# Performance work log

Hardware: AMD Instinct MI355X
Metric: run time of the kernel (lower is better)

## Reference

```python
import jax, jax.numpy as jnp
import numpy as np

N_NODES = 100000
N_EDGES = 3200000
F_IN = 256
HID = 64
N_CLS = 16


def setup_inputs() -> dict:
    key = jax.random.key(0)
    ks = jax.random.split(key, 12)
    x = jax.random.normal(ks[0], (N_NODES, F_IN), dtype=jnp.float32)
    edge_index = jax.random.randint(ks[1], (2, N_EDGES), 0, N_NODES, dtype=jnp.int32)
    w_mul = jax.random.normal(ks[2], (N_EDGES, 1), dtype=jnp.float32)
    s1 = 1.0 / np.sqrt(F_IN)
    s2 = 1.0 / np.sqrt(HID)
    # layer 1 params
    lin1_w = jax.random.uniform(ks[3], (HID, F_IN), minval=-s1, maxval=s1, dtype=jnp.float32)
    lin1_b = jax.random.uniform(ks[4], (HID,), minval=-s1, maxval=s1, dtype=jnp.float32)
    mlp1_w0 = jax.random.uniform(ks[5], (HID, 1), minval=-1.0, maxval=1.0, dtype=jnp.float32)
    mlp1_w1 = jax.random.uniform(ks[6], (HID, HID), minval=-s2, maxval=s2, dtype=jnp.float32)
    mlp1_b1 = jax.random.uniform(ks[7], (HID,), minval=-s2, maxval=s2, dtype=jnp.float32)
    # layer 2 params
    lin2_w = jax.random.uniform(ks[8], (N_CLS, HID), minval=-s2, maxval=s2, dtype=jnp.float32)
    lin2_b = jax.random.uniform(ks[9], (N_CLS,), minval=-s2, maxval=s2, dtype=jnp.float32)
    mlp2_w0 = jax.random.uniform(ks[10], (HID, 1), minval=-1.0, maxval=1.0, dtype=jnp.float32)
    mlp2_w1 = jax.random.uniform(ks[11], (N_CLS, HID), minval=-s2, maxval=s2, dtype=jnp.float32)
    mlp2_b1 = jnp.zeros((N_CLS,), dtype=jnp.float32)
    return dict(x=x, edge_index=edge_index, w_mul=w_mul,
                lin1_w=lin1_w, lin1_b=lin1_b, mlp1_w0=mlp1_w0, mlp1_w1=mlp1_w1, mlp1_b1=mlp1_b1,
                lin2_w=lin2_w, lin2_b=lin2_b, mlp2_w0=mlp2_w0, mlp2_w1=mlp2_w1, mlp2_b1=mlp2_b1)


def curv_layer(x, src, dst, w_mul, lin_w, lin_b, m_w0, m_w1, m_b1, n_nodes):
    # dense projection: [N, out]
    h = x @ lin_w.T + lin_b
    # per-edge weight MLP: Linear(1,HID,no bias) -> LeakyReLU(0.2) -> Linear(HID,out,bias)
    ew = jax.nn.leaky_relu(w_mul @ m_w0.T, negative_slope=0.2) @ m_w1.T + m_b1  # [E, out]
    # segment softmax keyed by source node (PyG softmax(out_weight, edge_index[0]))
    emax = jax.ops.segment_max(ew, src, num_segments=n_nodes)  # [N, out]
    e = jnp.exp(ew - emax[src])
    esum = jax.ops.segment_sum(e, src, num_segments=n_nodes)
    alpha = e / (esum[src] + 1e-16)  # [E, out]
    # message = alpha * x_j (x_j = h[src]); scatter-add at destination
    msg = alpha * h[src]
    return jax.ops.segment_sum(msg, dst, num_segments=n_nodes)  # [N, out]


def reference(x, edge_index, w_mul,
              lin1_w, lin1_b, mlp1_w0, mlp1_w1, mlp1_b1,
              lin2_w, lin2_b, mlp2_w0, mlp2_w1, mlp2_b1):
    src, dst = edge_index[0], edge_index[1]
    n = x.shape[0]
    # eval mode: dropout(p=0.8) is identity
    h = curv_layer(x, src, dst, w_mul, lin1_w, lin1_b, mlp1_w0, mlp1_w1, mlp1_b1, n)
    h = jax.nn.elu(h)
    h = curv_layer(h, src, dst, w_mul, lin2_w, lin2_b, mlp2_w0, mlp2_w1, mlp2_b1, n)
    return jax.nn.log_softmax(h, axis=1)
```

## Files before the change

kernel.cpp:

```cpp
#include <hip/hip_runtime.h>
#include <math.h>

#define FIN 256
#define HID 64
#define NCLS 16
#define BSH 8
#define BWD (1 << BSH)
#define NBKMAX 512
#define CAP 9216
#define CHUNK_S 8192
#define CHUNK_D 4096

typedef __attribute__((ext_vector_type(8))) short bf16x8;
typedef __attribute__((ext_vector_type(4))) float f32x4;

__global__ __launch_bounds__(512) void init_kernel(int* gcur_s, int* gcur_d) {
    int tid = threadIdx.x;
    gcur_s[tid] = tid * CAP;
    gcur_d[tid] = tid * CAP;
}

__global__ __launch_bounds__(512) void stage_kernel(const int* __restrict__ ei,
                                                    const float* __restrict__ w,
                                                    int* gcur_s, int* gcur_d,
                                                    unsigned int* st_s, uint2* st_d,
                                                    int E, int nchunk_s) {
    __shared__ int lh[NBKMAX];
    __shared__ int lofs[NBKMAX];
    __shared__ int lcur[NBKMAX];
    __shared__ int gbase[NBKMAX];
    __shared__ int wsum[8];
    __shared__ uint2 buf2[CHUNK_D];
    unsigned int* buf1 = (unsigned int*)buf2;
    int tid = threadIdx.x;
    int wv = tid >> 6, lane = tid & 63;
    int side = (blockIdx.x >= nchunk_s) ? 1 : 0;
    lh[tid] = 0;
    __syncthreads();
    if (!side) {
        int base = blockIdx.x * CHUNK_S;
        #pragma unroll
        for (int j = 0; j < CHUNK_S / 512; j++) {
            int e = base + tid + j * 512;
            if (e < E) atomicAdd(&lh[((unsigned)ei[e]) >> BSH], 1);
        }
    } else {
        int base = (blockIdx.x - nchunk_s) * CHUNK_D;
        #pragma unroll
        for (int j = 0; j < CHUNK_D / 512; j++) {
            int e = base + tid + j * 512;
            if (e < E) atomicAdd(&lh[((unsigned)ei[E + e]) >> BSH], 1);
        }
    }
    __syncthreads();
    int v = lh[tid];
    int inc = v;
    #pragma unroll
    for (int off = 1; off < 64; off <<= 1) {
        int p = __shfl_up(inc, off);
        if (lane >= off) inc += p;
    }
    if (lane == 63) wsum[wv] = inc;
    __syncthreads();
    int pre = 0;
    #pragma unroll
    for (int j = 0; j < 8; j++) pre += (j < wv) ? wsum[j] : 0;
    int ex = pre + inc - v;
    lofs[tid] = ex;
    lcur[tid] = ex;
    __syncthreads();
    if (!side) {
        int base = blockIdx.x * CHUNK_S;
        #pragma unroll
        for (int j = 0; j < CHUNK_S / 512; j++) {
            int e = base + tid + j * 512;
            if (e < E) {
                int s = ei[e];
                unsigned int rec = (__float_as_uint(w[e]) & 0xFFFFFF00u) | (unsigned int)(s & 0xFF);
                int p = atomicAdd(&lcur[((unsigned)s) >> BSH], 1);
                buf1[p] = rec;
            }
        }
    } else {
        int base = (blockIdx.x - nchunk_s) * CHUNK_D;
        #pragma unroll
        for (int j = 0; j < CHUNK_D / 512; j++) {
            int e = base + tid + j * 512;
            if (e < E) {
                int d = ei[E + e];
                int s = ei[e];
                unsigned int rec = (__float_as_uint(w[e]) & 0xFFFFFF00u) | (unsigned int)(d & 0xFF);
                int p = atomicAdd(&lcur[((unsigned)d) >> BSH], 1);
                buf2[p] = make_uint2((unsigned int)s, rec);
            }
        }
    }
    __syncthreads();
    {
        int c = lh[tid];
        if (c) gbase[tid] = atomicAdd(side ? &gcur_d[tid] : &gcur_s[tid], c);
    }
    __syncthreads();
    int sub = lane >> 4, ln = lane & 15;
    if (!side) {
        for (int b0 = wv * 64; b0 < wv * 64 + 64; b0 += 4) {
            int b = b0 + sub;
            int c = lh[b];
            int ls = lofs[b], gs = gbase[b];
            for (int i = ln; i < c; i += 16) st_s[gs + i] = buf1[ls + i];
        }
    } else {
        for (int b0 = wv * 64; b0 < wv * 64 + 64; b0 += 4) {
            int b = b0 + sub;
            int c = lh[b];
            int ls = lofs[b], gs = gbase[b];
            for (int i = ln; i < c; i += 16) st_d[gs + i] = buf2[ls + i];
        }
    }
}

__global__ __launch_bounds__(512) void bucket_scan_kernel(const int* gcur_s, const int* gcur_d,
                                                          int* bbase_s, int* bbase_d,
                                                          int* offs_s, int* offs_d,
                                                          int N, int nbk, int E) {
    int side = blockIdx.x;
    const int* gc = side ? gcur_d : gcur_s;
    int* bb = side ? bbase_d : bbase_s;
    __shared__ int tmp[512];
    int tid = threadIdx.x;
    int v = (tid < nbk) ? (gc[tid] - tid * CAP) : 0;
    tmp[tid] = v;
    __syncthreads();
    for (int off = 1; off < 512; off <<= 1) {
        int add = (tid >= off) ? tmp[tid - off] : 0;
        __syncthreads();
        tmp[tid] += add;
        __syncthreads();
    }
    if (tid < nbk) bb[tid] = tmp[tid] - v;
    if (tid == 0) {
        bb[nbk] = E;
        (side ? offs_d : offs_s)[N] = E;
    }
}

__global__ __launch_bounds__(512) void bucket_build_kernel(const int* __restrict__ bbase_s,
                                                           const int* __restrict__ bbase_d,
                                                           const unsigned int* __restrict__ st_s,
                                                           const uint2* __restrict__ st_d,
                                                           int* offs_s, int* mid_s, int* offs_d,
                                                           float* t_s, int2* ed, int N, int nbk) {
    __shared__ int lh[2 * BWD];
    __shared__ int lcur[2 * BWD];
    __shared__ int wsum[4];
    __shared__ int2 buf[CAP];
    int tid = threadIdx.x;
    int lane = tid & 63, wv = tid >> 6;
    int sside = (blockIdx.x < nbk);
    int b = sside ? blockIdx.x : (blockIdx.x - nbk);
    const int* bbase = sside ? bbase_s : bbase_d;
    int r0 = bbase[b];
    int cnt = bbase[b + 1] - r0;
    if (cnt > CAP) cnt = CAP;
    size_t sb = (size_t)b * CAP;
    int n0 = b << BSH;
    int nn = min(BWD, N - n0);
    lh[tid] = 0;
    __syncthreads();
    if (sside) {
        for (int i = tid; i < cnt; i += 512) {
            unsigned int rec = st_s[sb + i];
            atomicAdd(&lh[((rec & 0xFFu) << 1) | (rec >> 31)], 1);
        }
    } else {
        for (int i = tid; i < cnt; i += 512) {
            atomicAdd(&lh[st_d[sb + i].y & 0xFFu], 1);
        }
    }
    __syncthreads();
    int c0 = 0, v = 0, inc = 0;
    if (tid < 256) {
        if (sside) { c0 = lh[2 * tid]; v = c0 + lh[2 * tid + 1]; }
        else { v = lh[tid]; }
        inc = v;
        #pragma unroll
        for (int off = 1; off < 64; off <<= 1) {
            int p = __shfl_up(inc, off);
            if (lane >= off) inc += p;
        }
        if (lane == 63) wsum[wv] = inc;
    }
    __syncthreads();
    if (tid < 256) {
        int pre = 0;
        #pragma unroll
        for (int j = 0; j < 4; j++) pre += (j < wv) ? wsum[j] : 0;
        int ex = pre + inc - v;
        if (sside) {
            if (tid < nn) { offs_s[n0 + tid] = r0 + ex; mid_s[n0 + tid] = r0 + ex + c0; }
            lcur[2 * tid] = ex;
            lcur[2 * tid + 1] = ex + c0;
        } else {
            if (tid < nn) offs_d[n0 + tid] = r0 + ex;
            lcur[tid] = ex;
        }
    }
    __syncthreads();
    if (sside) {
        float* buff = (float*)buf;
        for (int i = tid; i < cnt; i += 512) {
            unsigned int rec = st_s[sb + i];
            int p = atomicAdd(&lcur[((rec & 0xFFu) << 1) | (rec >> 31)], 1);
            buff[p] = __uint_as_float(rec & 0xFFFFFF00u);
        }
        __syncthreads();
        for (int i = tid; i < cnt; i += 512) t_s[r0 + i] = buff[i];
    } else {
        for (int i = tid; i < cnt; i += 512) {
            uint2 rec = st_d[sb + i];
            int p = atomicAdd(&lcur[rec.y & 0xFFu], 1);
            buf[p] = make_int2((int)rec.x, (int)(rec.y & 0xFFFFFF00u));
        }
        __syncthreads();
        for (int i = tid; i < cnt; i += 512) ed[r0 + i] = buf[i];
    }
}

#define LOG2E 1.44269504088896340736f
__global__ void prep_kernel(const float* __restrict__ w0a, const float* __restrict__ w1a,
                            const float* __restrict__ w0b, const float* __restrict__ w1b,
                            float* Ap1, float* An1, float* Ap2, float* An2) {
    int tid = threadIdx.x;
    if (tid < 64) {
        float ap = 0.f, an = 0.f;
        for (int j = 0; j < 64; j++) {
            float w0 = w0a[j];
            float w1 = w1a[tid * 64 + j];
            ap += w0 * ((w0 >= 0.f) ? 1.f : 0.2f) * w1;
            an += w0 * ((w0 <= 0.f) ? 1.f : 0.2f) * w1;
        }
        Ap1[tid] = ap * LOG2E; An1[tid] = an * LOG2E;
    } else if (tid < 80) {
        int k = tid - 64;
        float ap = 0.f, an = 0.f;
        for (int j = 0; j < 64; j++) {
            float w0 = w0b[j];
            float w1 = w1b[k * 64 + j];
            ap += w0 * ((w0 >= 0.f) ? 1.f : 0.2f) * w1;
            an += w0 * ((w0 <= 0.f) ? 1.f : 0.2f) * w1;
        }
        Ap2[k] = ap * LOG2E; An2[k] = an * LOG2E;
    }
}

__device__ __forceinline__ float seg_expsum(const float* __restrict__ t, int i0, int i1, float a) {
    float sum = 0.f;
    int i = i0;
    for (; i + 3 < i1; i += 4) {
        float t0 = t[i], t1 = t[i + 1], t2 = t[i + 2], t3 = t[i + 3];
        sum += __builtin_amdgcn_exp2f(t0 * a);
        sum += __builtin_amdgcn_exp2f(t1 * a);
        sum += __builtin_amdgcn_exp2f(t2 * a);
        sum += __builtin_amdgcn_exp2f(t3 * a);
    }
    for (; i < i1; i++) sum += __builtin_amdgcn_exp2f(t[i] * a);
    return sum;
}

__global__ __launch_bounds__(256) void esum_kernel(const int* __restrict__ offs,
                                                   const int* __restrict__ mid,
                                                   const float* __restrict__ t_s,
                                                   const float* __restrict__ Ap1,
                                                   const float* __restrict__ An1,
                                                   const float* __restrict__ Ap2,
                                                   const float* __restrict__ An2,
                                                   float* __restrict__ inv1,
                                                   float* __restrict__ inv2, int N, int nblk1) {
    if ((int)blockIdx.x < nblk1) {
        int node = blockIdx.x * 4 + (threadIdx.x >> 6);
        int k = threadIdx.x & 63;
        if (node >= N) return;
        int s0 = offs[node], m = mid[node], s1 = offs[node + 1];
        float sum = seg_expsum(t_s, s0, m, Ap1[k]) + seg_expsum(t_s, m, s1, An1[k]);
        inv1[(size_t)node * 64 + k] = (s1 > s0) ? 1.f / (sum + 1e-16f) : 0.f;
    } else {
        int node = (blockIdx.x - nblk1) * 16 + (threadIdx.x >> 4);
        int k = threadIdx.x & 15;
        if (node >= N) return;
        int s0 = offs[node], m = mid[node], s1 = offs[node + 1];
        float sum = seg_expsum(t_s, s0, m, Ap2[k]) + seg_expsum(t_s, m, s1, An2[k]);
        inv2[(size_t)node * 16 + k] = (s1 > s0) ? 1.f / (sum + 1e-16f) : 0.f;
    }
}

__device__ __forceinline__ unsigned int bf16rn(float f) {
    unsigned int u = __float_as_uint(f);
    return (u + 0x7fffu + ((u >> 16) & 1u)) >> 16;
}

__device__ __forceinline__ void cvt8_split(const float4 a, const float4 b, bf16x8& h, bf16x8& l) {
    float f[8] = {a.x, a.y, a.z, a.w, b.x, b.y, b.z, b.w};
    #pragma unroll
    for (int j = 0; j < 8; j++) {
        unsigned int uh = bf16rn(f[j]);
        float hf = __uint_as_float(uh << 16);
        float r = f[j] - hf;
        unsigned int ul = bf16rn(r);
        h[j] = (short)uh;
        l[j] = (short)ul;
    }
}

#define KCH 64
__global__ __launch_bounds__(256, 4) void gemm1_kernel(const float* __restrict__ x,
                                                       const float* __restrict__ W,
                                                       const float* __restrict__ b,
                                                       const float* __restrict__ inv,
                                                       uint2* __restrict__ g1, int N) {
    __shared__ unsigned short xh[64 * KCH];
    __shared__ unsigned short xl[64 * KCH];
    __shared__ unsigned short wh[64 * KCH];
    __shared__ unsigned short wl[64 * KCH];
    int tid = threadIdx.x;
    int block_row = blockIdx.x * 64;
    float4 pf[4][2];
    auto load_chunk = [&](int kbase) {
        #pragma unroll
        for (int i = 0; i < 4; i++) {
            int t = tid + i * 256;
            if (t < 512) {
                int r = t >> 3, g = t & 7;
                int gr = block_row + r;
                if (gr < N) {
                    const float* p = &x[(size_t)gr * FIN + kbase + g * 8];
                    pf[i][0] = *(const float4*)p;
                    pf[i][1] = *(const float4*)(p + 4);
                } else {
                    pf[i][0] = make_float4(0.f, 0.f, 0.f, 0.f);
                    pf[i][1] = make_float4(0.f, 0.f, 0.f, 0.f);
                }
            } else {
                int r = (t - 512) >> 3, g = t & 7;
                const float* p = &W[r * FIN + kbase + g * 8];
                pf[i][0] = *(const float4*)p;
                pf[i][1] = *(const float4*)(p + 4);
            }
        }
    };
    auto write_chunk = [&]() {
        #pragma unroll
        for (int i = 0; i < 4; i++) {
            int t = tid + i * 256;
            int r = (t & 511) >> 3, g = t & 7;
            int gs = g ^ (r & 7);
            bf16x8 h, l;
            cvt8_split(pf[i][0], pf[i][1], h, l);
            if (t < 512) {
                *(bf16x8*)&xh[r * KCH + gs * 8] = h;
                *(bf16x8*)&xl[r * KCH + gs * 8] = l;
            } else {
                *(bf16x8*)&wh[r * KCH + gs * 8] = h;
                *(bf16x8*)&wl[r * KCH + gs * 8] = l;
            }
        }
    };

    int wv = tid >> 6, l = tid & 63;
    int lrow = l & 15, kg = l >> 4;
    f32x4 acc[4];
    #pragma unroll
    for (int c = 0; c < 4; c++) acc[c] = (f32x4){0.f, 0.f, 0.f, 0.f};

    const unsigned short* xrow_h = &xh[(wv * 16 + lrow) * KCH];
    const unsigned short* xrow_l = &xl[(wv * 16 + lrow) * KCH];

    load_chunk(0);
    for (int kc = 0; kc < FIN / KCH; kc++) {
        write_chunk();
        __syncthreads();
        if (kc + 1 < FIN / KCH) load_chunk((kc + 1) * KCH);
        #pragma unroll
        for (int s = 0; s < 2; s++) {
            int gB = ((s * 4 + kg) ^ (lrow & 7)) * 8;
            bf16x8 bh = *(const bf16x8*)&xrow_h[gB];
            bf16x8 bl = *(const bf16x8*)&xrow_l[gB];
            #pragma unroll
            for (int c = 0; c < 4; c++) {
                int wro = (c * 16 + lrow) * KCH + gB;
                bf16x8 ah = *(const bf16x8*)&wh[wro];
                bf16x8 al = *(const bf16x8*)&wl[wro];
                acc[c] = __builtin_amdgcn_mfma_f32_16x16x32_bf16(ah, bh, acc[c], 0, 0, 0);
                acc[c] = __builtin_amdgcn_mfma_f32_16x16x32_bf16(ah, bl, acc[c], 0, 0, 0);
                acc[c] = __builtin_amdgcn_mfma_f32_16x16x32_bf16(al, bh, acc[c], 0, 0, 0);
            }
        }
        __syncthreads();
    }
    int node = block_row + wv * 16 + lrow;
    if (node < N) {
        #pragma unroll
        for (int c = 0; c < 4; c++) {
            int colb = c * 16 + kg * 4;
            float4 bv = *(const float4*)&b[colb];
            float4 iv = *(const float4*)&inv[(size_t)node * 64 + colb];
            float o0 = (acc[c].x + bv.x) * iv.x;
            float o1 = (acc[c].y + bv.y) * iv.y;
            float o2 = (acc[c].z + bv.z) * iv.z;
            float o3 = (acc[c].w + bv.w) * iv.w;
            uint2 p;
            p.x = bf16rn(o0) | (bf16rn(o1) << 16);
            p.y = bf16rn(o2) | (bf16rn(o3) << 16);
            g1[(size_t)node * 16 + (colb >> 2)] = p;
        }
    }
}

#define GP 68
__global__ __launch_bounds__(256) void agg1g2_kernel(const int* __restrict__ offs,
                                                     const int2* __restrict__ ed,
                                                     const float* __restrict__ Ap,
                                                     const float* __restrict__ An,
                                                     const uint4* __restrict__ g,
                                                     const float* __restrict__ W2,
                                                     const float* __restrict__ b2,
                                                     const float* __restrict__ inv2,
                                                     float* __restrict__ g2, int N) {
    __shared__ float xs[32][GP];
    __shared__ float ws[16][GP];
    __shared__ float bs[16];
    int tid = threadIdx.x;
    {
        int c = tid >> 4, j4 = tid & 15;
        float4 v = ((const float4*)W2)[tid];
        ws[c][j4 * 4 + 0] = v.x; ws[c][j4 * 4 + 1] = v.y;
        ws[c][j4 * 4 + 2] = v.z; ws[c][j4 * 4 + 3] = v.w;
    }
    if (tid < 16) bs[tid] = b2[tid];

    int node0 = blockIdx.x * 32;
    int nl8 = tid >> 3;
    int node = node0 + nl8;
    int l = tid & 7;
    float4 acc0 = make_float4(0.f, 0.f, 0.f, 0.f);
    float4 acc1 = make_float4(0.f, 0.f, 0.f, 0.f);
    if (node < N) {
        int d0 = offs[node], d1 = offs[node + 1];
        float4 ap0 = ((const float4*)Ap)[l * 2], ap1 = ((const float4*)Ap)[l * 2 + 1];
        float4 an0 = ((const float4*)An)[l * 2], an1 = ((const float4*)An)[l * 2 + 1];
        int i = d0;
        int end4 = d0 + ((d1 - d0) & ~3);
        for (; i < end4; i += 4) {
            int2 e[4];
            #pragma unroll
            for (int j = 0; j < 4; j++) e[j] = ed[i + j];
            uint4 gv[4];
            #pragma unroll
            for (int j = 0; j < 4; j++)
                gv[j] = g[((size_t)e[j].x << 3) + l];
            #pragma unroll
            for (int j = 0; j < 4; j++) {
                float t = __int_as_float(e[j].y);
                float4 a0 = (t >= 0.f) ? ap0 : an0;
                float4 a1 = (t >= 0.f) ? ap1 : an1;
                acc0.x += __builtin_amdgcn_exp2f(t * a0.x) * __uint_as_float(gv[j].x << 16);
                acc0.y += __builtin_amdgcn_exp2f(t * a0.y) * __uint_as_float(gv[j].x & 0xffff0000u);
                acc0.z += __builtin_amdgcn_exp2f(t * a0.z) * __uint_as_float(gv[j].y << 16);
                acc0.w += __builtin_amdgcn_exp2f(t * a0.w) * __uint_as_float(gv[j].y & 0xffff0000u);
                acc1.x += __builtin_amdgcn_exp2f(t * a1.x) * __uint_as_float(gv[j].z << 16);
                acc1.y += __builtin_amdgcn_exp2f(t * a1.y) * __uint_as_float(gv[j].z & 0xffff0000u);
                acc1.z += __builtin_amdgcn_exp2f(t * a1.z) * __uint_as_float(gv[j].w << 16);
                acc1.w += __builtin_amdgcn_exp2f(t * a1.w) * __uint_as_float(gv[j].w & 0xffff0000u);
            }
        }
        for (; i < d1; i++) {
            int2 e = ed[i];
            float t = __int_as_float(e.y);
            float4 a0 = (t >= 0.f) ? ap0 : an0;
            float4 a1 = (t >= 0.f) ? ap1 : an1;
            uint4 gv = g[((size_t)e.x << 3) + l];
            acc0.x += __builtin_amdgcn_exp2f(t * a0.x) * __uint_as_float(gv.x << 16);
            acc0.y += __builtin_amdgcn_exp2f(t * a0.y) * __uint_as_float(gv.x & 0xffff0000u);
            acc0.z += __builtin_amdgcn_exp2f(t * a0.z) * __uint_as_float(gv.y << 16);
            acc0.w += __builtin_amdgcn_exp2f(t * a0.w) * __uint_as_float(gv.y & 0xffff0000u);
            acc1.x += __builtin_amdgcn_exp2f(t * a1.x) * __uint_as_float(gv.z << 16);
            acc1.y += __builtin_amdgcn_exp2f(t * a1.y) * __uint_as_float(gv.z & 0xffff0000u);
            acc1.z += __builtin_amdgcn_exp2f(t * a1.z) * __uint_as_float(gv.w << 16);
            acc1.w += __builtin_amdgcn_exp2f(t * a1.w) * __uint_as_float(gv.w & 0xffff0000u);
        }
    }
    float4 o0, o1;
    o0.x = (acc0.x > 0.f) ? acc0.x : (__expf(acc0.x) - 1.f);
    o0.y = (acc0.y > 0.f) ? acc0.y : (__expf(acc0.y) - 1.f);
    o0.z = (acc0.z > 0.f) ? acc0.z : (__expf(acc0.z) - 1.f);
    o0.w = (acc0.w > 0.f) ? acc0.w : (__expf(acc0.w) - 1.f);
    o1.x = (acc1.x > 0.f) ? acc1.x : (__expf(acc1.x) - 1.f);
    o1.y = (acc1.y > 0.f) ? acc1.y : (__expf(acc1.y) - 1.f);
    o1.z = (acc1.z > 0.f) ? acc1.z : (__expf(acc1.z) - 1.f);
    o1.w = (acc1.w > 0.f) ? acc1.w : (__expf(acc1.w) - 1.f);
    *(float4*)&xs[nl8][l * 8] = o0;
    *(float4*)&xs[nl8][l * 8 + 4] = o1;
    __syncthreads();
    int col = tid & 15;
    #pragma unroll
    for (int h = 0; h < 2; h++) {
        int nl = (tid >> 4) + h * 16;
        int gn = node0 + nl;
        if (gn < N) {
            float acc = bs[col];
            #pragma unroll
            for (int j4 = 0; j4 < 16; j4++) {
                float4 xv = *(const float4*)&xs[nl][j4 * 4];
                float4 wv = *(const float4*)&ws[col][j4 * 4];
                acc += xv.x * wv.x + xv.y * wv.y + xv.z * wv.z + xv.w * wv.w;
            }
            g2[(size_t)gn * NCLS + col] = acc * inv2[(size_t)gn * NCLS + col];
        }
    }
}

__global__ __launch_bounds__(256) void agg2_kernel(const int* __restrict__ offs,
                                                   const int2* __restrict__ ed,
                                                   const float* __restrict__ Ap,
                                                   const float* __restrict__ An,
                                                   const float* __restrict__ g,
                                                   float* __restrict__ out, int N) {
    int node = blockIdx.x * 64 + (threadIdx.x >> 2);
    int l = threadIdx.x & 3;
    if (node >= N) return;
    int d0 = offs[node], d1 = offs[node + 1];
    float4 ap = ((const float4*)Ap)[l];
    float4 an = ((const float4*)An)[l];
    float4 acc = make_float4(0.f, 0.f, 0.f, 0.f);
    int i = d0;
    int end8 = d0 + ((d1 - d0) & ~7);
    for (; i < end8; i += 8) {
        int2 e[8];
        #pragma unroll
        for (int j = 0; j < 8; j++) e[j] = ed[i + j];
        float4 gv[8];
        #pragma unroll
        for (int j = 0; j < 8; j++)
            gv[j] = *(const float4*)(g + ((size_t)e[j].x << 4) + l * 4);
        #pragma unroll
        for (int j = 0; j < 8; j++) {
            float t = __int_as_float(e[j].y);
            float4 a = (t >= 0.f) ? ap : an;
            acc.x += __builtin_amdgcn_exp2f(t * a.x) * gv[j].x;
            acc.y += __builtin_amdgcn_exp2f(t * a.y) * gv[j].y;
            acc.z += __builtin_amdgcn_exp2f(t * a.z) * gv[j].z;
            acc.w += __builtin_amdgcn_exp2f(t * a.w) * gv[j].w;
        }
    }
    for (; i < d1; i++) {
        int2 e = ed[i];
        float t = __int_as_float(e.y);
        float4 a = (t >= 0.f) ? ap : an;
        float4 gv = *(const float4*)(g + ((size_t)e.x << 4) + l * 4);
        acc.x += __builtin_amdgcn_exp2f(t * a.x) * gv.x;
        acc.y += __builtin_amdgcn_exp2f(t * a.y) * gv.y;
        acc.z += __builtin_amdgcn_exp2f(t * a.z) * gv.z;
        acc.w += __builtin_amdgcn_exp2f(t * a.w) * gv.w;
    }
    float m = fmaxf(fmaxf(acc.x, acc.y), fmaxf(acc.z, acc.w));
    m = fmaxf(m, __shfl_xor(m, 1, 4));
    m = fmaxf(m, __shfl_xor(m, 2, 4));
    float s = __expf(acc.x - m) + __expf(acc.y - m) + __expf(acc.z - m) + __expf(acc.w - m);
    s += __shfl_xor(s, 1, 4);
    s += __shfl_xor(s, 2, 4);
    float lse = m + __logf(s);
    float4 o = make_float4(acc.x - lse, acc.y - lse, acc.z - lse, acc.w - lse);
    *(float4*)(out + ((size_t)node << 4) + l * 4) = o;
}

extern "C" void kernel_launch(void* const* d_in, const int* in_sizes, int n_in,
                              void* d_out, int out_size, void* d_ws, size_t ws_size,
                              hipStream_t stream) {
    const float* x      = (const float*)d_in[0];
    const int*   ei     = (const int*)d_in[1];
    const float* wmul   = (const float*)d_in[2];
    const float* lin1_w = (const float*)d_in[3];
    const float* lin1_b = (const float*)d_in[4];
    const float* m1w0   = (const float*)d_in[5];
    const float* m1w1   = (const float*)d_in[6];
    const float* lin2_w = (const float*)d_in[8];
    const float* lin2_b = (const float*)d_in[9];
    const float* m2w0   = (const float*)d_in[10];
    const float* m2w1   = (const float*)d_in[11];

    int N = in_sizes[0] / FIN;
    int E = in_sizes[1] / 2;
    int nbk = (N + BWD - 1) >> BSH;
    int nchunk_s = (E + CHUNK_S - 1) / CHUNK_S;
    int nchunk_d = (E + CHUNK_D - 1) / CHUNK_D;

    char* ws = (char*)d_ws;
    auto alloc = [&](size_t bytes) {
        char* p = ws;
        ws += (bytes + 255) & ~(size_t)255;
        return p;
    };
    int*   gcur_s  = (int*)alloc(NBKMAX * 4);
    int*   gcur_d  = (int*)alloc(NBKMAX * 4);
    int*   bbase_s = (int*)alloc((NBKMAX + 1) * 4);
    int*   bbase_d = (int*)alloc((NBKMAX + 1) * 4);
    float* Ap1     = (float*)alloc(64 * 4);
    float* An1     = (float*)alloc(64 * 4);
    float* Ap2     = (float*)alloc(16 * 4);
    float* An2     = (float*)alloc(16 * 4);
    int*   offs_s  = (int*)alloc((size_t)(N + 1) * 4);
    int*   offs_d  = (int*)alloc((size_t)(N + 1) * 4);
    int*   mid_s   = (int*)alloc((size_t)N * 4);
    float* t_s     = (float*)alloc((size_t)E * 4);
    int2*  ed      = (int2*)alloc((size_t)E * 8);
    char*  reg = ws;
    unsigned int* st_s = (unsigned int*)(reg);
    uint2*        st_d = (uint2*)(reg + (((size_t)nbk * CAP * 4 + 255) & ~(size_t)255));
    float* inv1 = (float*)(reg);
    char*  regB = reg + (((size_t)N * 64 * 4 + 255) & ~(size_t)255);
    uint2* g1   = (uint2*)(regB);
    float* inv2 = (float*)(regB + ((size_t)N * 16 * 8));
    float* g2   = (float*)(regB + ((size_t)N * 16 * 8) + ((size_t)N * 16 * 4));

    int nblk1 = (N + 3) / 4;
    int nblk2 = (N + 15) / 16;

    init_kernel<<<1, 512, 0, stream>>>(gcur_s, gcur_d);
    prep_kernel<<<1, 128, 0, stream>>>(m1w0, m1w1, m2w0, m2w1, Ap1, An1, Ap2, An2);
    stage_kernel<<<nchunk_s + nchunk_d, 512, 0, stream>>>(ei, wmul, gcur_s, gcur_d,
                                                          st_s, st_d, E, nchunk_s);
    bucket_scan_kernel<<<2, 512, 0, stream>>>(gcur_s, gcur_d, bbase_s, bbase_d,
                                              offs_s, offs_d, N, nbk, E);
    bucket_build_kernel<<<2 * nbk, 512, 0, stream>>>(bbase_s, bbase_d, st_s, st_d,
                                                     offs_s, mid_s, offs_d, t_s, ed, N, nbk);
    esum_kernel<<<nblk1 + nblk2, 256, 0, stream>>>(offs_s, mid_s, t_s, Ap1, An1, Ap2, An2,
                                                   inv1, inv2, N, nblk1);
    gemm1_kernel<<<(N + 63) / 64, 256, 0, stream>>>(x, lin1_w, lin1_b, inv1, g1, N);
    agg1g2_kernel<<<(N + 31) / 32, 256, 0, stream>>>(offs_d, ed, Ap1, An1, (const uint4*)g1,
                                                     lin2_w, lin2_b, inv2, g2, N);
    agg2_kernel<<<(N + 63) / 64, 256, 0, stream>>>(offs_d, ed, Ap2, An2, g2, (float*)d_out, N);
}
```

Before: 461.7 us.

## Fuse layer-1 softmax denominator computation into gemm1 via shared memory

The layer-1 per-node exp-sum reciprocal (64 channels) moves out of the separate esum kernel and into the gemm1 prologue. Each wave computes inverse sums for its 16 rows into a 16 KB shared-memory table, and the epilogue reads from it. This drops the N×64 inv1 global write and read. The cost is extra LDS per block, which may lower occupancy below the 4-block launch bound, and serial per-node work in the GEMM prologue, which only partly overlaps the first prefetch.

```diff
diff --git a/kernel.cpp b/kernel.cpp
--- a/kernel.cpp
+++ b/kernel.cpp
@@ -267,30 +267,18 @@
     return sum;
 }
 
-__global__ __launch_bounds__(256) void esum_kernel(const int* __restrict__ offs,
-                                                   const int* __restrict__ mid,
-                                                   const float* __restrict__ t_s,
-                                                   const float* __restrict__ Ap1,
-                                                   const float* __restrict__ An1,
-                                                   const float* __restrict__ Ap2,
-                                                   const float* __restrict__ An2,
-                                                   float* __restrict__ inv1,
-                                                   float* __restrict__ inv2, int N, int nblk1) {
-    if ((int)blockIdx.x < nblk1) {
-        int node = blockIdx.x * 4 + (threadIdx.x >> 6);
-        int k = threadIdx.x & 63;
-        if (node >= N) return;
-        int s0 = offs[node], m = mid[node], s1 = offs[node + 1];
-        float sum = seg_expsum(t_s, s0, m, Ap1[k]) + seg_expsum(t_s, m, s1, An1[k]);
-        inv1[(size_t)node * 64 + k] = (s1 > s0) ? 1.f / (sum + 1e-16f) : 0.f;
-    } else {
-        int node = (blockIdx.x - nblk1) * 16 + (threadIdx.x >> 4);
-        int k = threadIdx.x & 15;
-        if (node >= N) return;
-        int s0 = offs[node], m = mid[node], s1 = offs[node + 1];
-        float sum = seg_expsum(t_s, s0, m, Ap2[k]) + seg_expsum(t_s, m, s1, An2[k]);
-        inv2[(size_t)node * 16 + k] = (s1 > s0) ? 1.f / (sum + 1e-16f) : 0.f;
-    }
+__global__ __launch_bounds__(256) void esum2_kernel(const int* __restrict__ offs,
+                                                    const int* __restrict__ mid,
+                                                    const float* __restrict__ t_s,
+                                                    const float* __restrict__ Ap,
+                                                    const float* __restrict__ An,
+                                                    float* __restrict__ inv, int N) {
+    int node = blockIdx.x * 16 + (threadIdx.x >> 4);
+    int k = threadIdx.x & 15;
+    if (node >= N) return;
+    int s0 = offs[node], m = mid[node], s1 = offs[node + 1];
+    float sum = seg_expsum(t_s, s0, m, Ap[k]) + seg_expsum(t_s, m, s1, An[k]);
+    inv[(size_t)node * 16 + k] = (s1 > s0) ? 1.f / (sum + 1e-16f) : 0.f;
 }
 
 __device__ __forceinline__ unsigned int bf16rn(float f) {
@@ -315,12 +303,17 @@
 __global__ __launch_bounds__(256, 4) void gemm1_kernel(const float* __restrict__ x,
                                                        const float* __restrict__ W,
                                                        const float* __restrict__ b,
-                                                       const float* __restrict__ inv,
+                                                       const int* __restrict__ offs,
+                                                       const int* __restrict__ mid,
+                                                       const float* __restrict__ t_s,
+                                                       const float* __restrict__ Ap,
+                                                       const float* __restrict__ An,
                                                        uint2* __restrict__ g1, int N) {
     __shared__ unsigned short xh[64 * KCH];
     __shared__ unsigned short xl[64 * KCH];
     __shared__ unsigned short wh[64 * KCH];
     __shared__ unsigned short wl[64 * KCH];
+    __shared__ float invl[64 * 64];
     int tid = threadIdx.x;
     int block_row = blockIdx.x * 64;
     float4 pf[4][2];
@@ -375,6 +368,19 @@
     const unsigned short* xrow_l = &xl[(wv * 16 + lrow) * KCH];
 
     load_chunk(0);
+    {
+        float ap = Ap[l], an = An[l];
+        for (int nn = 0; nn < 16; nn++) {
+            int nd = block_row + wv * 16 + nn;
+            float r = 0.f;
+            if (nd < N) {
+                int s0 = offs[nd], m = mid[nd], s1 = offs[nd + 1];
+                float sum = seg_expsum(t_s, s0, m, ap) + seg_expsum(t_s, m, s1, an);
+                r = (s1 > s0) ? 1.f / (sum + 1e-16f) : 0.f;
+            }
+            invl[(wv * 16 + nn) * 64 + l] = r;
+        }
+    }
     for (int kc = 0; kc < FIN / KCH; kc++) {
         write_chunk();
         __syncthreads();
@@ -402,7 +408,7 @@
         for (int c = 0; c < 4; c++) {
             int colb = c * 16 + kg * 4;
             float4 bv = *(const float4*)&b[colb];
-            float4 iv = *(const float4*)&inv[(size_t)node * 64 + colb];
+            float4 iv = *(const float4*)&invl[(wv * 16 + lrow) * 64 + colb];
             float o0 = (acc[c].x + bv.x) * iv.x;
             float o1 = (acc[c].y + bv.y) * iv.y;
             float o2 = (acc[c].z + bv.z) * iv.z;
@@ -615,14 +621,10 @@
     char*  reg = ws;
     unsigned int* st_s = (unsigned int*)(reg);
     uint2*        st_d = (uint2*)(reg + (((size_t)nbk * CAP * 4 + 255) & ~(size_t)255));
-    float* inv1 = (float*)(reg);
     char*  regB = reg + (((size_t)N * 64 * 4 + 255) & ~(size_t)255);
     uint2* g1   = (uint2*)(regB);
     float* inv2 = (float*)(regB + ((size_t)N * 16 * 8));
     float* g2   = (float*)(regB + ((size_t)N * 16 * 8) + ((size_t)N * 16 * 4));
-
-    int nblk1 = (N + 3) / 4;
-    int nblk2 = (N + 15) / 16;
 
     init_kernel<<<1, 512, 0, stream>>>(gcur_s, gcur_d);
     prep_kernel<<<1, 128, 0, stream>>>(m1w0, m1w1, m2w0, m2w1, Ap1, An1, Ap2, An2);
@@ -632,9 +634,9 @@
                                               offs_s, offs_d, N, nbk, E);
     bucket_build_kernel<<<2 * nbk, 512, 0, stream>>>(bbase_s, bbase_d, st_s, st_d,
                                                      offs_s, mid_s, offs_d, t_s, ed, N, nbk);
-    esum_kernel<<<nblk1 + nblk2, 256, 0, stream>>>(offs_s, mid_s, t_s, Ap1, An1, Ap2, An2,
-                                                   inv1, inv2, N, nblk1);
-    gemm1_kernel<<<(N + 63) / 64, 256, 0, stream>>>(x, lin1_w, lin1_b, inv1, g1, N);
+    esum2_kernel<<<(N + 15) / 16, 256, 0, stream>>>(offs_s, mid_s, t_s, Ap2, An2, inv2, N);
+    gemm1_kernel<<<(N + 63) / 64, 256, 0, stream>>>(x, lin1_w, lin1_b, offs_s, mid_s, t_s,
+                                                    Ap1, An1, g1, N);
     agg1g2_kernel<<<(N + 31) / 32, 256, 0, stream>>>(offs_d, ed, Ap1, An1, (const uint4*)g1,
                                                      lin2_w, lin2_b, inv2, g2, N);
     agg2_kernel<<<(N + 63) / 64, 256, 0, stream>>>(offs_d, ed, Ap2, An2, g2, (float*)d_out, N);
```

New measurement: 508.8 us. +10.2%, slower.
